# Performance work log

Hardware: AMD Instinct MI355X
Metric: run time of the kernel (lower is better)

Reference implementation:

```python
import jax, jax.numpy as jnp
import numpy as np

B, T, V, E, H, TAGS = 64, 256, 50000, 512, 512, 50


def _lstm_scan(xs, Wih, Whh, bih, bhh):
    # xs: [T, B, D]; torch LSTMCell gate order: i, f, g, o
    Bsz = xs.shape[1]
    Hd = Whh.shape[1]
    h0 = jnp.zeros((Bsz, Hd), xs.dtype)
    c0 = jnp.zeros((Bsz, Hd), xs.dtype)

    def step(carry, x_t):
        h, c = carry
        gates = x_t @ Wih.T + bih + h @ Whh.T + bhh  # [B, 4H]
        i, f, g, o = jnp.split(gates, 4, axis=-1)
        c = jax.nn.sigmoid(f) * c + jax.nn.sigmoid(i) * jnp.tanh(g)
        h = jax.nn.sigmoid(o) * jnp.tanh(c)
        return (h, c), h

    _, hs = jax.lax.scan(step, (h0, c0), xs)
    return hs  # [T, B, H]


def _bilstm_layer(xs, fw_params, bw_params):
    # xs: [T, B, D] -> [T, B, 2H]
    fw = _lstm_scan(xs, *fw_params)
    bw = _lstm_scan(xs[::-1], *bw_params)[::-1]
    return jnp.concatenate([fw, bw], axis=-1)


def setup_inputs() -> dict:
    key = jax.random.key(0)
    ks = iter(jax.random.split(key, 24))
    s = 0.05

    def p(shape):
        return (jax.random.normal(next(ks), shape, jnp.float32) * s)

    inp = {
        "x": jax.random.randint(next(ks), (B, T), 0, V),
        "lengths": jnp.full((B,), T, dtype=jnp.int32),
        "emb": p((V, E)),
        # layer 1 (input E)
        "Wih_f1": p((4 * H, E)), "Whh_f1": p((4 * H, H)), "bih_f1": p((4 * H,)), "bhh_f1": p((4 * H,)),
        "Wih_b1": p((4 * H, E)), "Whh_b1": p((4 * H, H)), "bih_b1": p((4 * H,)), "bhh_b1": p((4 * H,)),
        # layer 2 (input 2H)
        "Wih_f2": p((4 * H, 2 * H)), "Whh_f2": p((4 * H, H)), "bih_f2": p((4 * H,)), "bhh_f2": p((4 * H,)),
        "Wih_b2": p((4 * H, 2 * H)), "Whh_b2": p((4 * H, H)), "bih_b2": p((4 * H,)), "bhh_b2": p((4 * H,)),
        "fc_W": p((TAGS, 2 * H)), "fc_b": p((TAGS,)),
    }
    return inp


def reference(x, lengths, emb,
              Wih_f1, Whh_f1, bih_f1, bhh_f1,
              Wih_b1, Whh_b1, bih_b1, bhh_b1,
              Wih_f2, Whh_f2, bih_f2, bhh_f2,
              Wih_b2, Whh_b2, bih_b2, bhh_b2,
              fc_W, fc_b):
    embeds = emb[x]                      # [B, T, E]
    xs = embeds.transpose(1, 0, 2)       # [T, B, E]
    out1 = _bilstm_layer(xs, (Wih_f1, Whh_f1, bih_f1, bhh_f1),
                         (Wih_b1, Whh_b1, bih_b1, bhh_b1))  # [T, B, 2H]
    out2 = _bilstm_layer(out1, (Wih_f2, Whh_f2, bih_f2, bhh_f2),
                         (Wih_b2, Whh_b2, bih_b2, bhh_b2))  # [T, B, 2H]
    logits = out2 @ fc_W.T + fc_b        # [T, B, TAGS]
    return logits.transpose(1, 0, 2)     # [B, T, TAGS]
```

## Files before the change

### kernel.cpp

```cpp
#include <hip/hip_runtime.h>
#include <stdint.h>

typedef __attribute__((ext_vector_type(8))) short short8;
typedef __attribute__((ext_vector_type(4))) float f32x4;
typedef unsigned short bfraw;

#define Bn 64
#define Tn 256
#define En 512
#define Hn 512
#define TAGSn 50

__device__ __forceinline__ bfraw f2bf(float f) {
  union { float f; uint32_t u; } v; v.f = f;
  uint32_t u = v.u;
  return (bfraw)((u + 0x7FFFu + ((u >> 16) & 1u)) >> 16);
}
__device__ __forceinline__ float bf2f(bfraw h) {
  union { uint32_t u; float f; } v; v.u = ((uint32_t)h) << 16;
  return v.f;
}
__device__ __forceinline__ float sigm(float x) { return 1.f / (1.f + __expf(-x)); }
__device__ __forceinline__ float tanh_fast(float x) { return 1.f - 2.f / (__expf(2.f * x) + 1.f); }

__global__ void k_cvt(const float* __restrict__ s, bfraw* __restrict__ d, int n) {
  int i = blockIdx.x * 256 + threadIdx.x;
  if (i < n) d[i] = f2bf(s[i]);
}

__global__ void k_bias(const float* __restrict__ a, const float* __restrict__ b,
                       float* __restrict__ d, int n) {
  int i = blockIdx.x * 256 + threadIdx.x;
  if (i < n) d[i] = a[i] + b[i];
}

__global__ void k_fcpad(const float* __restrict__ w, const float* __restrict__ b,
                        bfraw* __restrict__ wd, float* __restrict__ bd) {
  int i = blockIdx.x * 256 + threadIdx.x;
  int row = i >> 10, col = i & 1023;
  wd[i] = (row < TAGSn) ? f2bf(w[row * 1024 + col]) : (bfraw)0;
  if (i < 128) bd[i] = (i < TAGSn) ? b[i] : 0.f;
}

__global__ void k_embed(const int* __restrict__ x, const float* __restrict__ emb,
                        bfraw* __restrict__ xs) {
  int i = blockIdx.x * 256 + threadIdx.x;
  int tok = i >> 6, c = i & 63;
  int t = tok >> 6, b = tok & 63;
  int vid = x[b * Tn + t];
  const float* src = emb + (size_t)vid * En + c * 8;
  float4 v0 = *(const float4*)(src);
  float4 v1 = *(const float4*)(src + 4);
  short8 o;
  o[0] = (short)f2bf(v0.x); o[1] = (short)f2bf(v0.y);
  o[2] = (short)f2bf(v0.z); o[3] = (short)f2bf(v0.w);
  o[4] = (short)f2bf(v1.x); o[5] = (short)f2bf(v1.y);
  o[6] = (short)f2bf(v1.z); o[7] = (short)f2bf(v1.w);
  *(short8*)(xs + (size_t)tok * En + c * 8) = o;
}

template <int MODE>
__global__ __launch_bounds__(256) void k_gemm(const bfraw* __restrict__ A,
                                              const bfraw* __restrict__ Bm,
                                              const float* __restrict__ bias,
                                              void* __restrict__ Cv, int K, int ldc, int rev) {
  __shared__ __align__(16) bfraw lA[128 * 64];
  __shared__ __align__(16) bfraw lB[128 * 64];
  const int tid = threadIdx.x;
  const int w = tid >> 6, l = tid & 63;
  const int wr = w >> 1, wc = w & 1;
  const size_t m0 = (size_t)blockIdx.x * 128;
  const size_t n0 = (size_t)blockIdx.y * 128;
  const int lr = l & 15;
  const int lk = (l >> 4) * 8;

  f32x4 acc[4][4];
#pragma unroll
  for (int i = 0; i < 4; i++)
#pragma unroll
    for (int jj = 0; jj < 4; jj++) acc[i][jj] = (f32x4){0.f, 0.f, 0.f, 0.f};

  for (int k0 = 0; k0 < K; k0 += 64) {
    short8 ra[4], rb[4];
#pragma unroll
    for (int c = 0; c < 4; c++) {
      int flat = c * 256 + tid;
      int row = flat >> 3, cc = flat & 7;
      ra[c] = *(const short8*)(A + (m0 + row) * K + k0 + cc * 8);
      rb[c] = *(const short8*)(Bm + (n0 + row) * K + k0 + cc * 8);
    }
    __syncthreads();
#pragma unroll
    for (int c = 0; c < 4; c++) {
      int flat = c * 256 + tid;
      int row = flat >> 3, cc = flat & 7;
      int off = row * 64 + ((cc * 8) ^ ((row & 7) << 3));
      *(short8*)(lA + off) = ra[c];
      *(short8*)(lB + off) = rb[c];
    }
    __syncthreads();
#pragma unroll
    for (int kk = 0; kk < 2; ++kk) {
      short8 aq[4], bq[4];
      int ks = kk * 32 + lk;
#pragma unroll
      for (int i = 0; i < 4; i++) {
        int row = wr * 64 + i * 16 + lr;
        aq[i] = *(const short8*)(lA + row * 64 + (ks ^ ((row & 7) << 3)));
      }
#pragma unroll
      for (int jj = 0; jj < 4; jj++) {
        int row = wc * 64 + jj * 16 + lr;
        bq[jj] = *(const short8*)(lB + row * 64 + (ks ^ ((row & 7) << 3)));
      }
#pragma unroll
      for (int i = 0; i < 4; i++)
#pragma unroll
        for (int jj = 0; jj < 4; jj++)
          acc[i][jj] = __builtin_amdgcn_mfma_f32_16x16x32_bf16(aq[i], bq[jj], acc[i][jj], 0, 0, 0);
    }
  }

  const int lq = (l >> 4) * 4;
#pragma unroll
  for (int i = 0; i < 4; i++)
#pragma unroll
    for (int jj = 0; jj < 4; jj++) {
#pragma unroll
      for (int r = 0; r < 4; r++) {
        size_t row = m0 + wr * 64 + i * 16 + lq + r;
        size_t col = n0 + wc * 64 + jj * 16 + lr;
        float v = acc[i][jj][r] + bias[col];
        if (MODE == 0) {
          size_t crow = rev ? ((size_t)(127 - (int)(row >> 6)) * 64 + (row & 63)) : row;
          ((bfraw*)Cv)[crow * ldc + col] = f2bf(v);
        } else {
          size_t tt = row >> 6, bb = row & 63;
          if ((int)col < TAGSn) ((float*)Cv)[(bb * Tn + tt) * TAGSn + col] = v;
        }
      }
    }
}

__global__ __launch_bounds__(256) void k_lstm_step(const bfraw* __restrict__ Gs,
                                                   const bfraw* __restrict__ Whh,
                                                   bfraw* __restrict__ out,
                                                   float* __restrict__ cbuf, int s, int srow) {
  __shared__ __align__(16) bfraw hl[64 * 512];
  __shared__ float gl[4 * 64 * 16];
  const int blk = blockIdx.x;
  const int d = blk >> 5, j = blk & 31;
  const int tid = threadIdx.x;
  const int w = tid >> 6, l = tid & 63;
  const int t = d ? (Tn - 1 - s) : s;
  const int tprev = d ? (t + 1) : (t - 1);

  if (s > 0) {
#pragma unroll
    for (int c = 0; c < 16; ++c) {
      int flat = c * 256 + tid;
      int row = flat >> 6;
      int cc = flat & 63;
      short8 v = *(const short8*)(out + (size_t)(tprev * Bn + row) * 1024 + d * 512 + cc * 8);
      *(short8*)(hl + row * 512 + ((cc * 8) ^ ((row & 7) << 3))) = v;
    }
  }
  __syncthreads();

  f32x4 acc[4];
#pragma unroll
  for (int i = 0; i < 4; i++) acc[i] = (f32x4){0.f, 0.f, 0.f, 0.f};

  if (s > 0) {
    const bfraw* Wd = Whh + ((size_t)d * 2048 + w * 512 + j * 16) * 512;
    const int lrr = l & 15, lk = (l >> 4) * 8;
#pragma unroll
    for (int kk = 0; kk < 16; ++kk) {
      short8 bq = *(const short8*)(Wd + (size_t)lrr * 512 + kk * 32 + lk);
#pragma unroll
      for (int mt = 0; mt < 4; ++mt) {
        int row = mt * 16 + lrr;
        int ks = kk * 32 + lk;
        short8 aq = *(const short8*)(hl + row * 512 + (ks ^ ((row & 7) << 3)));
        acc[mt] = __builtin_amdgcn_mfma_f32_16x16x32_bf16(aq, bq, acc[mt], 0, 0, 0);
      }
    }
  }

  {
    const int lrr = l & 15, lq = (l >> 4) * 4;
#pragma unroll
    for (int mt = 0; mt < 4; ++mt)
#pragma unroll
      for (int r = 0; r < 4; ++r) {
        int bb = mt * 16 + lq + r;
        float v = acc[mt][r] +
                  bf2f(Gs[(size_t)(srow * Bn + bb) * 4096 + d * 2048 + w * 512 + j * 16 + lrr]);
        gl[(w * 64 + bb) * 16 + lrr] = v;
      }
  }
  __syncthreads();

  {
    const int col = l & 15;
#pragma unroll
    for (int r = 0; r < 4; ++r) {
      int bb = w * 16 + (l >> 4) + r * 4;
      float vi = gl[(0 * 64 + bb) * 16 + col];
      float vf = gl[(1 * 64 + bb) * 16 + col];
      float vg = gl[(2 * 64 + bb) * 16 + col];
      float vo = gl[(3 * 64 + bb) * 16 + col];
      float* cp = cbuf + ((size_t)d * Bn + bb) * 512 + j * 16 + col;
      float c = (s > 0) ? *cp : 0.f;
      c = sigm(vf) * c + sigm(vi) * tanh_fast(vg);
      float h = sigm(vo) * tanh_fast(c);
      *cp = c;
      out[(size_t)(t * Bn + bb) * 1024 + d * 512 + j * 16 + col] = f2bf(h);
    }
  }
}

extern "C" void kernel_launch(void* const* d_in, const int* in_sizes, int n_in,
                              void* d_out, int out_size, void* d_ws, size_t ws_size,
                              hipStream_t stream) {
  const int*   x      = (const int*)d_in[0];
  const float* emb    = (const float*)d_in[2];
  const float* Wih_f1 = (const float*)d_in[3];
  const float* Whh_f1 = (const float*)d_in[4];
  const float* bih_f1 = (const float*)d_in[5];
  const float* bhh_f1 = (const float*)d_in[6];
  const float* Wih_b1 = (const float*)d_in[7];
  const float* Whh_b1 = (const float*)d_in[8];
  const float* bih_b1 = (const float*)d_in[9];
  const float* bhh_b1 = (const float*)d_in[10];
  const float* Wih_f2 = (const float*)d_in[11];
  const float* Whh_f2 = (const float*)d_in[12];
  const float* bih_f2 = (const float*)d_in[13];
  const float* bhh_f2 = (const float*)d_in[14];
  const float* Wih_b2 = (const float*)d_in[15];
  const float* Whh_b2 = (const float*)d_in[16];
  const float* bih_b2 = (const float*)d_in[17];
  const float* bhh_b2 = (const float*)d_in[18];
  const float* fc_W   = (const float*)d_in[19];
  const float* fc_b   = (const float*)d_in[20];

  char* ws = (char*)d_ws;
  bfraw* Wcat1 = (bfraw*)(ws + 0);
  bfraw* Whh1  = (bfraw*)(ws + 4194304);
  bfraw* Wcat2 = (bfraw*)(ws + 8388608);
  bfraw* Whh2  = (bfraw*)(ws + 16777216);
  bfraw* fcW   = (bfraw*)(ws + 20971520);
  float* bias1 = (float*)(ws + 21233664);
  float* bias2 = (float*)(ws + 21250048);
  float* fcb   = (float*)(ws + 21266432);
  float* cbuf  = (float*)(ws + 21266944);
  bfraw* out1  = (bfraw*)(ws + 22020096);
  bfraw* out2  = (bfraw*)(ws + 56623104);
  bfraw* xs    = out2;
  bfraw* Gs    = (bfraw*)(ws + 92274688);
  float* outp  = (float*)d_out;

  auto cvt = [&](const float* s, bfraw* dp, int n) {
    k_cvt<<<(n + 255) / 256, 256, 0, stream>>>(s, dp, n);
  };
  cvt(Wih_f1, Wcat1, 2048 * 512);
  cvt(Wih_b1, Wcat1 + 2048 * 512, 2048 * 512);
  cvt(Whh_f1, Whh1, 2048 * 512);
  cvt(Whh_b1, Whh1 + 2048 * 512, 2048 * 512);
  cvt(Wih_f2, Wcat2, 2048 * 1024);
  cvt(Wih_b2, Wcat2 + 2048 * 1024, 2048 * 1024);
  cvt(Whh_f2, Whh2, 2048 * 512);
  cvt(Whh_b2, Whh2 + 2048 * 512, 2048 * 512);
  k_bias<<<8, 256, 0, stream>>>(bih_f1, bhh_f1, bias1, 2048);
  k_bias<<<8, 256, 0, stream>>>(bih_b1, bhh_b1, bias1 + 2048, 2048);
  k_bias<<<8, 256, 0, stream>>>(bih_f2, bhh_f2, bias2, 2048);
  k_bias<<<8, 256, 0, stream>>>(bih_b2, bhh_b2, bias2 + 2048, 2048);
  k_fcpad<<<512, 256, 0, stream>>>(fc_W, fc_b, fcW, fcb);

  k_embed<<<4096, 256, 0, stream>>>(x, emb, xs);

  auto run_layer = [&](const bfraw* inL, int K, const bfraw* Wcat, const float* biasv,
                       const bfraw* WhhL, bfraw* outL) {
    for (int c = 0; c < 2; ++c) {
      k_gemm<0><<<dim3(64, 16), 256, 0, stream>>>(
          inL + (size_t)c * 8192 * K, Wcat, biasv, Gs, K, 4096, 0);
      k_gemm<0><<<dim3(64, 16), 256, 0, stream>>>(
          inL + (size_t)(1 - c) * 8192 * K, Wcat + (size_t)2048 * K, biasv + 2048,
          Gs + 2048, K, 4096, 1);
      for (int s = c * 128; s < c * 128 + 128; ++s)
        k_lstm_step<<<64, 256, 0, stream>>>(Gs, WhhL, outL, cbuf, s, s - c * 128);
    }
  };

  run_layer(xs, 512, Wcat1, bias1, Whh1, out1);
  run_layer(out1, 1024, Wcat2, bias2, Whh2, out2);

  k_gemm<1><<<dim3(128, 1), 256, 0, stream>>>(out2, fcW, fcb, outp, 1024, 0, 0);
}
```

Before: 4.160 ms.

## Replace per-step LSTM launches with persistent kernel using grid-wide atomic barrier

Replaces the 256 per-timestep kernel launches per layer with one persistent kernel of 64 blocks that loops over all timesteps and synchronizes across blocks through an atomic counter spin-wait. Recurrent weights are held in registers for the whole sequence, and the cell state moves from a global buffer into registers. The input-projection GEMM now covers the full sequence in one launch per direction instead of two chunked halves with reversed row mapping, which needs a larger gate buffer. This removes launch overhead and repeated weight reloads, but relies on all 64 blocks being co-resident and adds spin-wait latency plus register pressure.

```diff
diff --git a/kernel.cpp b/kernel.cpp
--- a/kernel.cpp
+++ b/kernel.cpp
@@ -63,7 +63,7 @@
 __global__ __launch_bounds__(256) void k_gemm(const bfraw* __restrict__ A,
                                               const bfraw* __restrict__ Bm,
                                               const float* __restrict__ bias,
-                                              void* __restrict__ Cv, int K, int ldc, int rev) {
+                                              void* __restrict__ Cv, int K, int ldc) {
   __shared__ __align__(16) bfraw lA[128 * 64];
   __shared__ __align__(16) bfraw lB[128 * 64];
   const int tid = threadIdx.x;
@@ -132,8 +132,7 @@
         size_t col = n0 + wc * 64 + jj * 16 + lr;
         float v = acc[i][jj][r] + bias[col];
         if (MODE == 0) {
-          size_t crow = rev ? ((size_t)(127 - (int)(row >> 6)) * 64 + (row & 63)) : row;
-          ((bfraw*)Cv)[crow * ldc + col] = f2bf(v);
+          ((bfraw*)Cv)[row * ldc + col] = f2bf(v);
         } else {
           size_t tt = row >> 6, bb = row & 63;
           if ((int)col < TAGSn) ((float*)Cv)[(bb * Tn + tt) * TAGSn + col] = v;
@@ -142,81 +141,102 @@
     }
 }
 
-__global__ __launch_bounds__(256) void k_lstm_step(const bfraw* __restrict__ Gs,
-                                                   const bfraw* __restrict__ Whh,
-                                                   bfraw* __restrict__ out,
-                                                   float* __restrict__ cbuf, int s, int srow) {
+__global__ __launch_bounds__(256) void k_lstm_seq(const bfraw* __restrict__ G,
+                                                  const bfraw* __restrict__ Whh,
+                                                  bfraw* __restrict__ out,
+                                                  int* __restrict__ bar) {
   __shared__ __align__(16) bfraw hl[64 * 512];
   __shared__ float gl[4 * 64 * 16];
   const int blk = blockIdx.x;
   const int d = blk >> 5, j = blk & 31;
   const int tid = threadIdx.x;
   const int w = tid >> 6, l = tid & 63;
-  const int t = d ? (Tn - 1 - s) : s;
-  const int tprev = d ? (t + 1) : (t - 1);
-
-  if (s > 0) {
-#pragma unroll
-    for (int c = 0; c < 16; ++c) {
-      int flat = c * 256 + tid;
-      int row = flat >> 6;
-      int cc = flat & 63;
-      short8 v = *(const short8*)(out + (size_t)(tprev * Bn + row) * 1024 + d * 512 + cc * 8);
-      *(short8*)(hl + row * 512 + ((cc * 8) ^ ((row & 7) << 3))) = v;
-    }
+  const int lr = l & 15, lk = (l >> 4) * 8, lq = (l >> 4) * 4;
+  int* cnt = bar + d;
+
+  short8 bq[16];
+  {
+    const bfraw* Wd = Whh + ((size_t)(d * 2048 + w * 512 + j * 16 + lr)) * 512;
+#pragma unroll
+    for (int kk = 0; kk < 16; ++kk) bq[kk] = *(const short8*)(Wd + kk * 32 + lk);
   }
-  __syncthreads();
-
-  f32x4 acc[4];
-#pragma unroll
-  for (int i = 0; i < 4; i++) acc[i] = (f32x4){0.f, 0.f, 0.f, 0.f};
-
-  if (s > 0) {
-    const bfraw* Wd = Whh + ((size_t)d * 2048 + w * 512 + j * 16) * 512;
-    const int lrr = l & 15, lk = (l >> 4) * 8;
-#pragma unroll
-    for (int kk = 0; kk < 16; ++kk) {
-      short8 bq = *(const short8*)(Wd + (size_t)lrr * 512 + kk * 32 + lk);
-#pragma unroll
-      for (int mt = 0; mt < 4; ++mt) {
-        int row = mt * 16 + lrr;
-        int ks = kk * 32 + lk;
-        short8 aq = *(const short8*)(hl + row * 512 + (ks ^ ((row & 7) << 3)));
-        acc[mt] = __builtin_amdgcn_mfma_f32_16x16x32_bf16(aq, bq, acc[mt], 0, 0, 0);
-      }
-    }
-  }
-
-  {
-    const int lrr = l & 15, lq = (l >> 4) * 4;
+
+  float creg[4] = {0.f, 0.f, 0.f, 0.f};
+
+  for (int s = 0; s < Tn; ++s) {
+    const int t = d ? (Tn - 1 - s) : s;
+    const int tprev = d ? (t + 1) : (t - 1);
+
+    float gpre[4][4];
 #pragma unroll
     for (int mt = 0; mt < 4; ++mt)
 #pragma unroll
       for (int r = 0; r < 4; ++r) {
         int bb = mt * 16 + lq + r;
-        float v = acc[mt][r] +
-                  bf2f(Gs[(size_t)(srow * Bn + bb) * 4096 + d * 2048 + w * 512 + j * 16 + lrr]);
-        gl[(w * 64 + bb) * 16 + lrr] = v;
-      }
-  }
-  __syncthreads();
-
-  {
-    const int col = l & 15;
+        gpre[mt][r] =
+            bf2f(G[((size_t)t * Bn + bb) * 4096 + d * 2048 + w * 512 + j * 16 + lr]);
+      }
+
+    if (s > 0) {
+      if (tid == 0) {
+        while (__hip_atomic_load(cnt, __ATOMIC_ACQUIRE, __HIP_MEMORY_SCOPE_AGENT) < 32 * s)
+          __builtin_amdgcn_s_sleep(2);
+      }
+      __syncthreads();
+#pragma unroll
+      for (int c = 0; c < 16; ++c) {
+        int flat = c * 256 + tid;
+        int row = flat >> 6, cc = flat & 63;
+        short8 v = *(const short8*)(out + ((size_t)tprev * Bn + row) * 1024 + d * 512 + cc * 8);
+        *(short8*)(hl + row * 512 + ((cc * 8) ^ ((row & 7) << 3))) = v;
+      }
+      __syncthreads();
+    }
+
+    f32x4 acc[4];
+#pragma unroll
+    for (int i = 0; i < 4; i++) acc[i] = (f32x4){0.f, 0.f, 0.f, 0.f};
+
+    if (s > 0) {
+#pragma unroll
+      for (int kk = 0; kk < 16; ++kk) {
+        int ks = kk * 32 + lk;
+#pragma unroll
+        for (int mt = 0; mt < 4; ++mt) {
+          int row = mt * 16 + lr;
+          short8 aq = *(const short8*)(hl + row * 512 + (ks ^ ((row & 7) << 3)));
+          acc[mt] = __builtin_amdgcn_mfma_f32_16x16x32_bf16(aq, bq[kk], acc[mt], 0, 0, 0);
+        }
+      }
+    }
+
+#pragma unroll
+    for (int mt = 0; mt < 4; ++mt)
+#pragma unroll
+      for (int r = 0; r < 4; ++r) {
+        int bb = mt * 16 + lq + r;
+        gl[(w * 64 + bb) * 16 + lr] = acc[mt][r] + gpre[mt][r];
+      }
+    __syncthreads();
+
 #pragma unroll
     for (int r = 0; r < 4; ++r) {
       int bb = w * 16 + (l >> 4) + r * 4;
+      int col = l & 15;
       float vi = gl[(0 * 64 + bb) * 16 + col];
       float vf = gl[(1 * 64 + bb) * 16 + col];
       float vg = gl[(2 * 64 + bb) * 16 + col];
       float vo = gl[(3 * 64 + bb) * 16 + col];
-      float* cp = cbuf + ((size_t)d * Bn + bb) * 512 + j * 16 + col;
-      float c = (s > 0) ? *cp : 0.f;
-      c = sigm(vf) * c + sigm(vi) * tanh_fast(vg);
-      float h = sigm(vo) * tanh_fast(c);
-      *cp = c;
-      out[(size_t)(t * Bn + bb) * 1024 + d * 512 + j * 16 + col] = f2bf(h);
-    }
+      float cv = creg[r];
+      cv = sigm(vf) * cv + sigm(vi) * tanh_fast(vg);
+      float h = sigm(vo) * tanh_fast(cv);
+      creg[r] = cv;
+      out[((size_t)t * Bn + bb) * 1024 + d * 512 + j * 16 + col] = f2bf(h);
+    }
+
+    __syncthreads();
+    if (tid == 0)
+      __hip_atomic_fetch_add(cnt, 1, __ATOMIC_RELEASE, __HIP_MEMORY_SCOPE_AGENT);
   }
 }
 
@@ -253,12 +273,14 @@
   float* bias1 = (float*)(ws + 21233664);
   float* bias2 = (float*)(ws + 21250048);
   float* fcb   = (float*)(ws + 21266432);
-  float* cbuf  = (float*)(ws + 21266944);
+  int*   bar   = (int*)(ws + 21266944);
   bfraw* out1  = (bfraw*)(ws + 22020096);
   bfraw* out2  = (bfraw*)(ws + 56623104);
   bfraw* xs    = out2;
-  bfraw* Gs    = (bfraw*)(ws + 92274688);
+  bfraw* G     = (bfraw*)(ws + 92274688);
   float* outp  = (float*)d_out;
+
+  hipMemsetAsync(bar, 0, 64, stream);
 
   auto cvt = [&](const float* s, bfraw* dp, int n) {
     k_cvt<<<(n + 255) / 256, 256, 0, stream>>>(s, dp, n);
@@ -279,21 +301,15 @@
 
   k_embed<<<4096, 256, 0, stream>>>(x, emb, xs);
 
-  auto run_layer = [&](const bfraw* inL, int K, const bfraw* Wcat, const float* biasv,
-                       const bfraw* WhhL, bfraw* outL) {
-    for (int c = 0; c < 2; ++c) {
-      k_gemm<0><<<dim3(64, 16), 256, 0, stream>>>(
-          inL + (size_t)c * 8192 * K, Wcat, biasv, Gs, K, 4096, 0);
-      k_gemm<0><<<dim3(64, 16), 256, 0, stream>>>(
-          inL + (size_t)(1 - c) * 8192 * K, Wcat + (size_t)2048 * K, biasv + 2048,
-          Gs + 2048, K, 4096, 1);
-      for (int s = c * 128; s < c * 128 + 128; ++s)
-        k_lstm_step<<<64, 256, 0, stream>>>(Gs, WhhL, outL, cbuf, s, s - c * 128);
-    }
-  };
-
-  run_layer(xs, 512, Wcat1, bias1, Whh1, out1);
-  run_layer(out1, 1024, Wcat2, bias2, Whh2, out2);
-
-  k_gemm<1><<<dim3(128, 1), 256, 0, stream>>>(out2, fcW, fcb, outp, 1024, 0, 0);
-}
+  k_gemm<0><<<dim3(128, 16), 256, 0, stream>>>(xs, Wcat1, bias1, G, 512, 4096);
+  k_gemm<0><<<dim3(128, 16), 256, 0, stream>>>(xs, Wcat1 + 2048 * 512, bias1 + 2048,
+                                               G + 2048, 512, 4096);
+  k_lstm_seq<<<64, 256, 0, stream>>>(G, Whh1, out1, bar);
+
+  k_gemm<0><<<dim3(128, 16), 256, 0, stream>>>(out1, Wcat2, bias2, G, 1024, 4096);
+  k_gemm<0><<<dim3(128, 16), 256, 0, stream>>>(out1, Wcat2 + (size_t)2048 * 1024,
+                                               bias2 + 2048, G + 2048, 1024, 4096);
+  k_lstm_seq<<<64, 256, 0, stream>>>(G, Whh2, out2, bar + 2);
+
+  k_gemm<1><<<dim3(128, 1), 256, 0, stream>>>(out2, fcW, fcb, outp, 1024, 0);
+}
```

After: 4.091 ms. Within noise of the previous version (-1.7%).
